# Optimization experiments

Measured on AMD Instinct MI355X. Metric: run time of the kernel, lower is better.

The kernel has to match this reference:

```python
import jax, jax.numpy as jnp
import numpy as np

HEADS = 8
DIM_HEAD = 64
INNER = HEADS * DIM_HEAD  # 512
EPS = 1e-6


def layer_norm(x, gamma, beta):
    mu = jnp.mean(x, axis=-1, keepdims=True)
    var = jnp.var(x, axis=-1, keepdims=True)
    return (x - mu) * jax.lax.rsqrt(var + EPS) * gamma + beta


def setup_inputs() -> dict:
    key = jax.random.key(0)
    ks = jax.random.split(key, 8)
    b, n = 2, 2048
    s = lambda d: 1.0 / np.sqrt(d)
    return {
        "x": jax.random.normal(ks[0], (b, n, INNER), dtype=jnp.float32),
        # weights stored input-major: y = x @ W
        "w_qkv": jax.random.normal(ks[1], (INNER, 3 * INNER), dtype=jnp.float32) * s(INNER),
        "w_out": jax.random.normal(ks[2], (INNER, INNER), dtype=jnp.float32) * s(INNER),
        "b_out": jax.random.normal(ks[3], (INNER,), dtype=jnp.float32) * 0.01,
        "w_ff1": jax.random.normal(ks[4], (INNER, 4 * INNER), dtype=jnp.float32) * s(INNER),
        "w_ff2": jax.random.normal(ks[5], (4 * INNER, INNER), dtype=jnp.float32) * s(4 * INNER),
        "g1": jnp.ones((INNER,), dtype=jnp.float32),
        "be1": jnp.zeros((INNER,), dtype=jnp.float32),
        "g2": jnp.ones((INNER,), dtype=jnp.float32),
        "be2": jnp.zeros((INNER,), dtype=jnp.float32),
    }


def reference(x, w_qkv, w_out, b_out, w_ff1, w_ff2, g1, be1, g2, be2):
    b, n, _ = x.shape
    scale = DIM_HEAD ** (-0.5)
    qkv = x @ w_qkv  # [b, n, 3*inner]
    qkv = qkv.reshape(b, n, 3, HEADS, DIM_HEAD)
    q = qkv[:, :, 0].transpose(0, 2, 1, 3)  # [b, h, n, d]
    k = qkv[:, :, 1].transpose(0, 2, 1, 3)
    v = qkv[:, :, 2].transpose(0, 2, 1, 3)
    dots = jnp.einsum('bhqd,bhkd->bhqk', q, k) * scale
    attn = jax.nn.softmax(dots, axis=-1)
    out = jnp.einsum('bhqk,bhkd->bhqd', attn, v)
    out = out.transpose(0, 2, 1, 3).reshape(b, n, INNER)
    out = out @ w_out + b_out
    attn_res = layer_norm(x + out, g1, be1)
    # NOTE: no activation between the two FFN linears (faithful to source)
    ff = (attn_res @ w_ff1) @ w_ff2
    return layer_norm(attn_res + ff, g2, be2)
```

## Files before the change

### kernel.cpp

```cpp
#include <hip/hip_runtime.h>
#include <hip/hip_bf16.h>
#include <cstdint>
#include <cstddef>
#include <math.h>

#define HEADS 8
#define DHEAD 64
#define INNER 512
#define BATCH 2
#define SEQ   2048
#define MROWS (BATCH*SEQ)
#define LN_EPS 1e-6f
#define KSPLIT 4
#define KCHUNK (SEQ/KSPLIT)

typedef unsigned short u16;
typedef __attribute__((ext_vector_type(8))) short short8;
typedef __attribute__((ext_vector_type(4))) short short4v;
typedef __attribute__((ext_vector_type(4))) float f32x4;

#define MFMA16(a,b,c) __builtin_amdgcn_mfma_f32_16x16x32_bf16((a),(b),(c),0,0,0)
#if __has_builtin(__builtin_amdgcn_mfma_f32_16x16x16bf16_1k)
#define HAVE_MFMA16K16 1
#define MFMA16K16(a,b,c) __builtin_amdgcn_mfma_f32_16x16x16bf16_1k((a),(b),(c),0,0,0)
#endif

__device__ __forceinline__ float bf2f(u16 u) {
    union { float f; uint32_t i; } x; x.i = ((uint32_t)u) << 16; return x.f;
}
__device__ __forceinline__ u16 f2bf(float f) {
    __hip_bfloat16 h = __float2bfloat16(f);
    return *reinterpret_cast<u16*>(&h);
}
__device__ __forceinline__ void gl_lds16(const void* g, void* l) {
    __builtin_amdgcn_global_load_lds(
        (const __attribute__((address_space(1))) void*)g,
        (__attribute__((address_space(3))) void*)l, 16, 0, 0);
}

__global__ void prep_kernel(const float* __restrict__ x, u16* __restrict__ x_b,
                            const float* __restrict__ w_qkv, u16* __restrict__ w_qkvT,
                            const float* __restrict__ w_out, u16* __restrict__ w_outT,
                            const float* __restrict__ w_ff1, u16* __restrict__ w_ff1T,
                            const float* __restrict__ w_ff2, u16* __restrict__ w_ff2T) {
    __shared__ float T[32][33];
    const int blk = blockIdx.x, tid = threadIdx.x;
    if (blk < 2048) {
        int i = blk * 256 + tid;
        float4 v = reinterpret_cast<const float4*>(x)[i];
        ushort4 o;
        o.x = f2bf(v.x); o.y = f2bf(v.y); o.z = f2bf(v.z); o.w = f2bf(v.w);
        reinterpret_cast<ushort4*>(x_b)[i] = o;
        return;
    }
    const float* B; u16* Bt; int K, N, t;
    if (blk < 2816)      { B = w_qkv; Bt = w_qkvT; K = 512;  N = 1536; t = blk - 2048; }
    else if (blk < 3072) { B = w_out; Bt = w_outT; K = 512;  N = 512;  t = blk - 2816; }
    else if (blk < 4096) { B = w_ff1; Bt = w_ff1T; K = 512;  N = 2048; t = blk - 3072; }
    else                 { B = w_ff2; Bt = w_ff2T; K = 2048; N = 512;  t = blk - 4096; }
    const int nb = N / 32;
    const int n0 = (t % nb) * 32, k0 = (t / nb) * 32;
    const int r = tid >> 3, c = (tid & 7) * 4;
    float4 v = *reinterpret_cast<const float4*>(&B[(size_t)(k0 + r) * N + n0 + c]);
    T[c + 0][r] = v.x; T[c + 1][r] = v.y; T[c + 2][r] = v.z; T[c + 3][r] = v.w;
    __syncthreads();
    ushort4 o;
    o.x = f2bf(T[r][c + 0]); o.y = f2bf(T[r][c + 1]);
    o.z = f2bf(T[r][c + 2]); o.w = f2bf(T[r][c + 3]);
    *reinterpret_cast<ushort4*>(&Bt[(size_t)(n0 + r) * K + k0 + c]) = o;
}

template<int BN, int EPI>
__global__ __launch_bounds__(256) void gemm_bt(const u16* __restrict__ A,
                                               const u16* __restrict__ Bt,
                                               u16* __restrict__ Cb,
                                               u16* __restrict__ Vt,
                                               int M, int N, int K) {
    constexpr int WN = BN / 2;
    constexpr int NT = WN / 16;
    __shared__ u16 As[128 * 32];
    __shared__ u16 Bs[BN * 32];
    const int tid = threadIdx.x;
    const int wave = tid >> 6, lane = tid & 63;
    const int l15 = lane & 15, quad = lane >> 4;
    const int wm = (wave >> 1) * 64, wn = (wave & 1) * WN;
    const int row0 = blockIdx.y * 128, col0 = blockIdx.x * BN;

    int kbase = 0, kend = K;
    if (EPI == 3) {
        int chunk = K / gridDim.z;
        kbase = blockIdx.z * chunk; kend = kbase + chunk;
    }

    f32x4 acc[4][NT];
    #pragma unroll
    for (int mi = 0; mi < 4; ++mi)
        #pragma unroll
        for (int ni = 0; ni < NT; ++ni)
            #pragma unroll
            for (int e = 0; e < 4; ++e) acc[mi][ni][e] = 0.f;

    for (int k0 = kbase; k0 < kend; k0 += 32) {
        #pragma unroll
        for (int idx0 = 0; idx0 < 512 + BN * 4; idx0 += 256) {
            int idx = idx0 + tid;
            if (idx < 512) {
                int r = idx >> 2, ic = (idx & 3) * 8;
                gl_lds16(A + (size_t)(row0 + r) * K + k0 + ic, &As[idx * 8]);
            } else {
                int ib = idx - 512;
                int r = ib >> 2, ic = (ib & 3) * 8;
                gl_lds16(Bt + (size_t)(col0 + r) * K + k0 + ic, &Bs[ib * 8]);
            }
        }
        __syncthreads();

        short8 af[4], bfr[NT];
        #pragma unroll
        for (int mi = 0; mi < 4; ++mi)
            af[mi] = *reinterpret_cast<const short8*>(&As[(wm + mi * 16 + l15) * 32 + quad * 8]);
        #pragma unroll
        for (int ni = 0; ni < NT; ++ni)
            bfr[ni] = *reinterpret_cast<const short8*>(&Bs[(wn + ni * 16 + l15) * 32 + quad * 8]);
        #pragma unroll
        for (int mi = 0; mi < 4; ++mi)
            #pragma unroll
            for (int ni = 0; ni < NT; ++ni)
                acc[mi][ni] = MFMA16(af[mi], bfr[ni], acc[mi][ni]);
        __syncthreads();
    }

    #pragma unroll
    for (int mi = 0; mi < 4; ++mi)
        #pragma unroll
        for (int ni = 0; ni < NT; ++ni) {
            const int cc = col0 + wn + ni * 16 + l15;
            const int rr0 = row0 + wm + mi * 16 + quad * 4;
            if (EPI == 0) {
                #pragma unroll
                for (int r = 0; r < 4; ++r)
                    Cb[(size_t)(rr0 + r) * N + cc] = f2bf(acc[mi][ni][r]);
            } else if (EPI == 3) {
                u16* Cz = Cb + (size_t)blockIdx.z * M * N;
                #pragma unroll
                for (int r = 0; r < 4; ++r)
                    Cz[(size_t)(rr0 + r) * N + cc] = f2bf(acc[mi][ni][r]);
            } else {
                if (cc < 1024) {
                    size_t base = (cc < 512) ? (size_t)cc
                                             : ((size_t)MROWS * 512 + cc - 512);
                    #pragma unroll
                    for (int r = 0; r < 4; ++r)
                        Cb[base + (size_t)(rr0 + r) * 512] = f2bf(acc[mi][ni][r]);
                } else {
                    int hh = (cc - 1024) >> 6, dd = (cc - 1024) & 63;
                    int bb = rr0 >> 11, srow = rr0 & 2047;
                    ushort4 o;
                    o.x = f2bf(acc[mi][ni][0]); o.y = f2bf(acc[mi][ni][1]);
                    o.z = f2bf(acc[mi][ni][2]); o.w = f2bf(acc[mi][ni][3]);
                    *reinterpret_cast<ushort4*>(
                        &Vt[(((size_t)(bb * 8 + hh) * 64 + dd) << 11) + srow]) = o;
                }
            }
        }
}

__global__ __launch_bounds__(256) void gemm_proj(const u16* __restrict__ OpartB,
                                                 const float* __restrict__ lpart,
                                                 const u16* __restrict__ Bt,
                                                 const float* __restrict__ bias,
                                                 float* __restrict__ C) {
    __shared__ u16 As[64 * 32];
    __shared__ u16 Bs[64 * 32];
    const int tid = threadIdx.x;
    const int wave = tid >> 6, lane = tid & 63;
    const int l15 = lane & 15, quad = lane >> 4;
    const int wm = (wave >> 1) * 32, wn = (wave & 1) * 32;
    const int row0 = blockIdx.y * 64, col0 = blockIdx.x * 64;

    f32x4 acc[2][2];
    #pragma unroll
    for (int mi = 0; mi < 2; ++mi)
        #pragma unroll
        for (int ni = 0; ni < 2; ++ni)
            #pragma unroll
            for (int e = 0; e < 4; ++e) acc[mi][ni][e] = 0.f;

    const int r = tid >> 2, ic = (tid & 3) * 8;
    const int gr = row0 + r;
    const int bb = gr >> 11, srow = gr & 2047;

    for (int k0 = 0; k0 < 512; k0 += 32) {
        gl_lds16(Bt + (size_t)(col0 + r) * 512 + k0 + ic, &Bs[tid * 8]);
        {
            const int gc = k0 + ic;
            const int h = gc >> 6, d0 = gc & 63;
            const int bh = bb * 8 + h;
            float l = 0.f, o[8] = {0.f, 0.f, 0.f, 0.f, 0.f, 0.f, 0.f, 0.f};
            #pragma unroll
            for (int ks = 0; ks < KSPLIT; ++ks) {
                size_t pk = ((size_t)(ks * 16 + bh) << 11) + srow;
                l += lpart[pk];
                uint4 uv = *reinterpret_cast<const uint4*>(&OpartB[pk * 64 + d0]);
                const u16* up = (const u16*)&uv;
                #pragma unroll
                for (int i = 0; i < 8; ++i) o[i] += bf2f(up[i]);
            }
            float inv = 1.f / l;
            u16 a8[8];
            #pragma unroll
            for (int i = 0; i < 8; ++i) a8[i] = f2bf(o[i] * inv);
            *reinterpret_cast<uint4*>(&As[tid * 8]) =
                *reinterpret_cast<const uint4*>(a8);
        }
        __syncthreads();

        short8 af[2], bfr[2];
        #pragma unroll
        for (int mi = 0; mi < 2; ++mi)
            af[mi] = *reinterpret_cast<const short8*>(&As[(wm + mi * 16 + l15) * 32 + quad * 8]);
        #pragma unroll
        for (int ni = 0; ni < 2; ++ni)
            bfr[ni] = *reinterpret_cast<const short8*>(&Bs[(wn + ni * 16 + l15) * 32 + quad * 8]);
        #pragma unroll
        for (int mi = 0; mi < 2; ++mi)
            #pragma unroll
            for (int ni = 0; ni < 2; ++ni)
                acc[mi][ni] = MFMA16(af[mi], bfr[ni], acc[mi][ni]);
        __syncthreads();
    }

    #pragma unroll
    for (int mi = 0; mi < 2; ++mi)
        #pragma unroll
        for (int ni = 0; ni < 2; ++ni) {
            const int cc = col0 + wn + ni * 16 + l15;
            const int rr0 = row0 + wm + mi * 16 + quad * 4;
            #pragma unroll
            for (int rr = 0; rr < 4; ++rr)
                C[(size_t)(rr0 + rr) * 512 + cc] = acc[mi][ni][rr] + bias[cc];
        }
}

__global__ __launch_bounds__(256) void attn_kernel(const u16* __restrict__ qk_b,
                                                   const u16* __restrict__ vT_b,
                                                   u16* __restrict__ OpartB,
                                                   float* __restrict__ lpart) {
    __shared__ u16 SM[64 * 64 + 2 * 64 * 72];
    u16 (*Qs)[64] = (u16(*)[64])SM;
    u16 (*Ks)[72] = (u16(*)[72])(SM + 64 * 64);
    u16 (*VT)[72] = (u16(*)[72])(SM + 64 * 64 + 64 * 72);

    const int tid = threadIdx.x;
    const int wave = tid >> 6, lane = tid & 63;
    const int l15 = lane & 15, quad = lane >> 4;
    const int qt = blockIdx.x, bh = blockIdx.y, ks = blockIdx.z;
    const int b = bh >> 3, h = bh & 7;
    const int w16 = wave * 16;
    const int r0 = tid >> 3, r1 = r0 + 32;
    const int ch = (tid & 7) * 8;

    {
        const u16* qb = qk_b + (size_t)(b * SEQ + qt * 64) * 512 + h * 64;
        *reinterpret_cast<uint4*>(&Qs[r0][ch]) =
            *reinterpret_cast<const uint4*>(&qb[(size_t)r0 * 512 + ch]);
        *reinterpret_cast<uint4*>(&Qs[r1][ch]) =
            *reinterpret_cast<const uint4*>(&qb[(size_t)r1 * 512 + ch]);
    }
    __syncthreads();

    short8 qf[2];
    qf[0] = *reinterpret_cast<const short8*>(&Qs[w16 + l15][quad * 8]);
    qf[1] = *reinterpret_cast<const short8*>(&Qs[w16 + l15][32 + quad * 8]);

    const u16* kb = qk_b + (size_t)MROWS * 512
                  + (size_t)(b * SEQ + ks * KCHUNK) * 512 + h * 64;
    const u16* vb = vT_b + (size_t)bh * 64 * 2048 + ks * KCHUNK;

    uint4 kr0 = *reinterpret_cast<const uint4*>(&kb[(size_t)r0 * 512 + ch]);
    uint4 kr1 = *reinterpret_cast<const uint4*>(&kb[(size_t)r1 * 512 + ch]);
    uint4 vr0 = *reinterpret_cast<const uint4*>(&vb[(size_t)r0 * 2048 + ch]);
    uint4 vr1 = *reinterpret_cast<const uint4*>(&vb[(size_t)r1 * 2048 + ch]);

    const float CEXP = 0.18033688011110918f;

#ifdef HAVE_MFMA16K16
    f32x4 oacc[4];
    float lsum = 0.f;
    #pragma unroll
    for (int di = 0; di < 4; ++di)
        #pragma unroll
        for (int e = 0; e < 4; ++e) oacc[di][e] = 0.f;

    for (int kt = 0; kt < KCHUNK / 64; ++kt) {
        *reinterpret_cast<uint4*>(&Ks[r0][ch]) = kr0;
        *reinterpret_cast<uint4*>(&Ks[r1][ch]) = kr1;
        *reinterpret_cast<uint4*>(&VT[r0][ch]) = vr0;
        *reinterpret_cast<uint4*>(&VT[r1][ch]) = vr1;
        __syncthreads();

        if (kt + 1 < KCHUNK / 64) {
            const u16* kb2 = kb + (size_t)(kt + 1) * 64 * 512;
            const u16* vb2 = vb + (kt + 1) * 64;
            kr0 = *reinterpret_cast<const uint4*>(&kb2[(size_t)r0 * 512 + ch]);
            kr1 = *reinterpret_cast<const uint4*>(&kb2[(size_t)r1 * 512 + ch]);
            vr0 = *reinterpret_cast<const uint4*>(&vb2[(size_t)r0 * 2048 + ch]);
            vr1 = *reinterpret_cast<const uint4*>(&vb2[(size_t)r1 * 2048 + ch]);
        }

        f32x4 sacc[4];
        #pragma unroll
        for (int ni = 0; ni < 4; ++ni)
            #pragma unroll
            for (int e = 0; e < 4; ++e) sacc[ni][e] = 0.f;
        #pragma unroll
        for (int ksk = 0; ksk < 2; ++ksk) {
            short8 kf[4];
            #pragma unroll
            for (int ni = 0; ni < 4; ++ni)
                kf[ni] = *reinterpret_cast<const short8*>(
                    &Ks[ni * 16 + l15][ksk * 32 + quad * 8]);
            #pragma unroll
            for (int ni = 0; ni < 4; ++ni)
                sacc[ni] = MFMA16(kf[ni], qf[ksk], sacc[ni]);
        }

        #pragma unroll
        for (int ni = 0; ni < 4; ++ni) {
            short4v pp;
            #pragma unroll
            for (int r = 0; r < 4; ++r) {
                float p = exp2f(sacc[ni][r] * CEXP);
                lsum += p;
                pp[r] = (short)f2bf(p);
            }
            #pragma unroll
            for (int di = 0; di < 4; ++di) {
                short4v vf = *reinterpret_cast<const short4v*>(
                    &VT[di * 16 + l15][ni * 16 + quad * 4]);
                oacc[di] = MFMA16K16(vf, pp, oacc[di]);
            }
        }
        __syncthreads();
    }

    lsum += __shfl_xor(lsum, 16);
    lsum += __shfl_xor(lsum, 32);

    const size_t pbase = ((size_t)(ks * 16 + bh) * SEQ + qt * 64);
    if (lane < 16) lpart[pbase + w16 + lane] = lsum;

    float* OTf = (float*)SM;
    #pragma unroll
    for (int di = 0; di < 4; ++di)
        #pragma unroll
        for (int r = 0; r < 4; ++r)
            OTf[(di * 16 + quad * 4 + r) * 68 + w16 + l15] = oacc[di][r];
    __syncthreads();

    const int ql = tid >> 2, dseg = (tid & 3) * 16;
    u16 ov[16];
    #pragma unroll
    for (int i = 0; i < 16; ++i) ov[i] = f2bf(OTf[(dseg + i) * 68 + ql]);
    u16* op = &OpartB[(pbase + ql) * 64 + dseg];
    *reinterpret_cast<uint4*>(op)     = *reinterpret_cast<const uint4*>(ov);
    *reinterpret_cast<uint4*>(op + 8) = *reinterpret_cast<const uint4*>(ov + 8);
#else
    f32x4 oacc[4];
    float lsum[4];
    #pragma unroll
    for (int di = 0; di < 4; ++di)
        #pragma unroll
        for (int e = 0; e < 4; ++e) oacc[di][e] = 0.f;
    #pragma unroll
    for (int r = 0; r < 4; ++r) lsum[r] = 0.f;

    for (int kt = 0; kt < KCHUNK / 64; ++kt) {
        *reinterpret_cast<uint4*>(&Ks[r0][ch]) = kr0;
        *reinterpret_cast<uint4*>(&Ks[r1][ch]) = kr1;
        *reinterpret_cast<uint4*>(&VT[r0][ch]) = vr0;
        *reinterpret_cast<uint4*>(&VT[r1][ch]) = vr1;
        __syncthreads();

        if (kt + 1 < KCHUNK / 64) {
            const u16* kb2 = kb + (size_t)(kt + 1) * 64 * 512;
            const u16* vb2 = vb + (kt + 1) * 64;
            kr0 = *reinterpret_cast<const uint4*>(&kb2[(size_t)r0 * 512 + ch]);
            kr1 = *reinterpret_cast<const uint4*>(&kb2[(size_t)r1 * 512 + ch]);
            vr0 = *reinterpret_cast<const uint4*>(&vb2[(size_t)r0 * 2048 + ch]);
            vr1 = *reinterpret_cast<const uint4*>(&vb2[(size_t)r1 * 2048 + ch]);
        }

        f32x4 sacc[4];
        #pragma unroll
        for (int ni = 0; ni < 4; ++ni)
            #pragma unroll
            for (int e = 0; e < 4; ++e) sacc[ni][e] = 0.f;
        #pragma unroll
        for (int ksk = 0; ksk < 2; ++ksk) {
            short8 kf[4];
            #pragma unroll
            for (int ni = 0; ni < 4; ++ni)
                kf[ni] = *reinterpret_cast<const short8*>(
                    &Ks[ni * 16 + l15][ksk * 32 + quad * 8]);
            #pragma unroll
            for (int ni = 0; ni < 4; ++ni)
                sacc[ni] = MFMA16(qf[ksk], kf[ni], sacc[ni]);
        }
        #pragma unroll
        for (int ni = 0; ni < 4; ++ni)
            #pragma unroll
            for (int r = 0; r < 4; ++r) {
                float p = exp2f(sacc[ni][r] * CEXP);
                lsum[r] += p;
                Qs[w16 + quad * 4 + r][ni * 16 + l15] = f2bf(p);
            }
        #pragma unroll
        for (int ksk = 0; ksk < 2; ++ksk) {
            short8 pf = *reinterpret_cast<const short8*>(
                &Qs[w16 + l15][ksk * 32 + quad * 8]);
            #pragma unroll
            for (int di = 0; di < 4; ++di) {
                short8 vf = *reinterpret_cast<const short8*>(
                    &VT[di * 16 + l15][ksk * 32 + quad * 8]);
                oacc[di] = MFMA16(pf, vf, oacc[di]);
            }
        }
        __syncthreads();
    }

    #pragma unroll
    for (int r = 0; r < 4; ++r) {
        float v = lsum[r];
        v += __shfl_xor(v, 1); v += __shfl_xor(v, 2);
        v += __shfl_xor(v, 4); v += __shfl_xor(v, 8);
        lsum[r] = v;
    }
    const size_t pbase = ((size_t)(ks * 16 + bh) * SEQ + qt * 64);
    #pragma unroll
    for (int di = 0; di < 4; ++di)
        #pragma unroll
        for (int r = 0; r < 4; ++r)
            OpartB[(pbase + w16 + quad * 4 + r) * 64 + di * 16 + l15] = f2bf(oacc[di][r]);
    if (l15 == 0)
        #pragma unroll
        for (int r = 0; r < 4; ++r)
            lpart[pbase + w16 + quad * 4 + r] = lsum[r];
#endif
}

template<bool A16, bool S16, bool TWO>
__global__ __launch_bounds__(256) void ln_kernel(const void* __restrict__ a_,
                                                 const void* __restrict__ s0_,
                                                 const void* __restrict__ s1_,
                                                 const float* __restrict__ g,
                                                 const float* __restrict__ be,
                                                 float* __restrict__ out32,
                                                 u16* __restrict__ out16) {
    const int tid = threadIdx.x, wave = tid >> 6, lane = tid & 63;
    const int row = blockIdx.x * 4 + wave;
    const size_t off = (size_t)row * INNER;

    float v[8];
    #pragma unroll
    for (int j = 0; j < 2; ++j) {
        const int c = j * 256 + lane * 4;
        float a0, a1, a2, a3;
        if (A16) {
            ushort4 u = *reinterpret_cast<const ushort4*>((const u16*)a_ + off + c);
            a0 = bf2f(u.x); a1 = bf2f(u.y); a2 = bf2f(u.z); a3 = bf2f(u.w);
        } else {
            float4 u = *reinterpret_cast<const float4*>((const float*)a_ + off + c);
            a0 = u.x; a1 = u.y; a2 = u.z; a3 = u.w;
        }
        float s0, s1, s2, s3;
        if (S16) {
            ushort4 u = *reinterpret_cast<const ushort4*>((const u16*)s0_ + off + c);
            s0 = bf2f(u.x); s1 = bf2f(u.y); s2 = bf2f(u.z); s3 = bf2f(u.w);
        } else {
            float4 u = *reinterpret_cast<const float4*>((const float*)s0_ + off + c);
            s0 = u.x; s1 = u.y; s2 = u.z; s3 = u.w;
        }
        v[j*4+0] = a0 + s0; v[j*4+1] = a1 + s1; v[j*4+2] = a2 + s2; v[j*4+3] = a3 + s3;
        if (TWO) {
            if (S16) {
                ushort4 u = *reinterpret_cast<const ushort4*>((const u16*)s1_ + off + c);
                v[j*4+0] += bf2f(u.x); v[j*4+1] += bf2f(u.y);
                v[j*4+2] += bf2f(u.z); v[j*4+3] += bf2f(u.w);
            } else {
                float4 u = *reinterpret_cast<const float4*>((const float*)s1_ + off + c);
                v[j*4+0] += u.x; v[j*4+1] += u.y; v[j*4+2] += u.z; v[j*4+3] += u.w;
            }
        }
    }

    float s = 0.f;
    #pragma unroll
    for (int i = 0; i < 8; ++i) s += v[i];
    #pragma unroll
    for (int m = 1; m < 64; m <<= 1) s += __shfl_xor(s, m);
    const float mu = s * (1.f / INNER);

    float q = 0.f;
    #pragma unroll
    for (int i = 0; i < 8; ++i) { v[i] -= mu; q += v[i] * v[i]; }
    #pragma unroll
    for (int m = 1; m < 64; m <<= 1) q += __shfl_xor(q, m);
    const float rstd = rsqrtf(q * (1.f / INNER) + LN_EPS);

    #pragma unroll
    for (int j = 0; j < 2; ++j) {
        const int c = j * 256 + lane * 4;
        float4 gv = *reinterpret_cast<const float4*>(g + c);
        float4 bv = *reinterpret_cast<const float4*>(be + c);
        float y0 = v[j*4+0] * rstd * gv.x + bv.x;
        float y1 = v[j*4+1] * rstd * gv.y + bv.y;
        float y2 = v[j*4+2] * rstd * gv.z + bv.z;
        float y3 = v[j*4+3] * rstd * gv.w + bv.w;
        if (out32) {
            float4 o = {y0, y1, y2, y3};
            *reinterpret_cast<float4*>(out32 + off + c) = o;
        }
        if (out16) {
            ushort4 o;
            o.x = f2bf(y0); o.y = f2bf(y1); o.z = f2bf(y2); o.w = f2bf(y3);
            *reinterpret_cast<ushort4*>(out16 + off + c) = o;
        }
    }
}

extern "C" void kernel_launch(void* const* d_in, const int* in_sizes, int n_in,
                              void* d_out, int out_size, void* d_ws, size_t ws_size,
                              hipStream_t stream) {
    const float* x     = (const float*)d_in[0];
    const float* w_qkv = (const float*)d_in[1];
    const float* w_out = (const float*)d_in[2];
    const float* b_out = (const float*)d_in[3];
    const float* w_ff1 = (const float*)d_in[4];
    const float* w_ff2 = (const float*)d_in[5];
    const float* g1    = (const float*)d_in[6];
    const float* be1   = (const float*)d_in[7];
    const float* g2    = (const float*)d_in[8];
    const float* be2   = (const float*)d_in[9];
    float* out = (float*)d_out;

    char* W = (char*)d_ws;
    u16*   w_outT     = (u16*)  (W + 0);
    u16*   w_ff1T     = (u16*)  (W + 524288);
    u16*   w_ff2T     = (u16*)  (W + 2621440);
    u16*   qk_b       = (u16*)  (W + 4718592);
    float* proj       = (float*)(W + 4718592);
    u16*   ff2p       = (u16*)  (W + 4718592);
    u16*   vT_b       = (u16*)  (W + 13107200);
    u16*   attn_res_b = (u16*)  (W + 13107200);
    u16*   x_b        = (u16*)  (W + 17301504);
    u16*   w_qkvT     = (u16*)  (W + 21495808);
    u16*   OpartB     = (u16*)  (W + 17301504);
    u16*   ff1_b      = (u16*)  (W + 17301504);
    float* lpart      = (float*)(W + 34078720);

    prep_kernel<<<5120, 256, 0, stream>>>(x, x_b, w_qkv, w_qkvT, w_out, w_outT,
                                          w_ff1, w_ff1T, w_ff2, w_ff2T);

    gemm_bt<64, 2><<<dim3(1536 / 64, MROWS / 128), 256, 0, stream>>>(
        x_b, w_qkvT, qk_b, vT_b, MROWS, 1536, INNER);

    attn_kernel<<<dim3(SEQ / 64, BATCH * HEADS, KSPLIT), 256, 0, stream>>>(
        qk_b, vT_b, OpartB, lpart);

    gemm_proj<<<dim3(INNER / 64, MROWS / 64), 256, 0, stream>>>(
        OpartB, lpart, w_outT, b_out, proj);

    ln_kernel<false, false, false><<<MROWS / 4, 256, 0, stream>>>(
        x, proj, nullptr, g1, be1, nullptr, attn_res_b);

    gemm_bt<128, 0><<<dim3(2048 / 128, MROWS / 128), 256, 0, stream>>>(
        attn_res_b, w_ff1T, ff1_b, nullptr, MROWS, 2048, INNER);

    gemm_bt<64, 3><<<dim3(INNER / 64, MROWS / 128, 2), 256, 0, stream>>>(
        ff1_b, w_ff2T, ff2p, nullptr, MROWS, INNER, 2048);

    ln_kernel<true, true, true><<<MROWS / 4, 256, 0, stream>>>(
        attn_res_b, ff2p, ff2p + (size_t)MROWS * INNER, g2, be2, out, nullptr);
}
```

Baseline: 233.1 us.

## Fold softmax scale into Q, split attention combine from output projection

Pre-multiplies Q by the softmax scale (log2e/sqrt(d)) in the QKV GEMM epilogue, so the attention kernel's exp2 no longer needs a multiply. The P-to-bf16 pack now uses byte-permute truncation, which rounds toward zero instead of to nearest. The fused combine+projection kernel, which recomputed the split-K merge for every column tile, becomes a separate elementwise combine kernel plus the generic 128-row GEMM with a bias epilogue. This adds a kernel launch and an extra bf16 intermediate round-trip, and slightly changes numerics.

```diff
diff --git a/kernel.cpp b/kernel.cpp
--- a/kernel.cpp
+++ b/kernel.cpp
@@ -13,6 +13,7 @@
 #define LN_EPS 1e-6f
 #define KSPLIT 4
 #define KCHUNK (SEQ/KSPLIT)
+#define QSCALE 0.18033688011110918f
 
 typedef unsigned short u16;
 typedef __attribute__((ext_vector_type(8))) short short8;
@@ -73,6 +74,8 @@
 template<int BN, int EPI>
 __global__ __launch_bounds__(256) void gemm_bt(const u16* __restrict__ A,
                                                const u16* __restrict__ Bt,
+                                               const float* __restrict__ bias,
+                                               float* __restrict__ C,
                                                u16* __restrict__ Cb,
                                                u16* __restrict__ Vt,
                                                int M, int N, int K) {
@@ -140,6 +143,10 @@
                 #pragma unroll
                 for (int r = 0; r < 4; ++r)
                     Cb[(size_t)(rr0 + r) * N + cc] = f2bf(acc[mi][ni][r]);
+            } else if (EPI == 1) {
+                #pragma unroll
+                for (int r = 0; r < 4; ++r)
+                    C[(size_t)(rr0 + r) * N + cc] = acc[mi][ni][r] + bias[cc];
             } else if (EPI == 3) {
                 u16* Cz = Cb + (size_t)blockIdx.z * M * N;
                 #pragma unroll
@@ -147,11 +154,13 @@
                     Cz[(size_t)(rr0 + r) * N + cc] = f2bf(acc[mi][ni][r]);
             } else {
                 if (cc < 1024) {
-                    size_t base = (cc < 512) ? (size_t)cc
-                                             : ((size_t)MROWS * 512 + cc - 512);
+                    const bool isq = (cc < 512);
+                    size_t base = isq ? (size_t)cc
+                                      : ((size_t)MROWS * 512 + cc - 512);
+                    const float sc = isq ? QSCALE : 1.f;
                     #pragma unroll
                     for (int r = 0; r < 4; ++r)
-                        Cb[base + (size_t)(rr0 + r) * 512] = f2bf(acc[mi][ni][r]);
+                        Cb[base + (size_t)(rr0 + r) * 512] = f2bf(acc[mi][ni][r] * sc);
                 } else {
                     int hh = (cc - 1024) >> 6, dd = (cc - 1024) & 63;
                     int bb = rr0 >> 11, srow = rr0 & 2047;
@@ -165,83 +174,6 @@
         }
 }
 
-__global__ __launch_bounds__(256) void gemm_proj(const u16* __restrict__ OpartB,
-                                                 const float* __restrict__ lpart,
-                                                 const u16* __restrict__ Bt,
-                                                 const float* __restrict__ bias,
-                                                 float* __restrict__ C) {
-    __shared__ u16 As[64 * 32];
-    __shared__ u16 Bs[64 * 32];
-    const int tid = threadIdx.x;
-    const int wave = tid >> 6, lane = tid & 63;
-    const int l15 = lane & 15, quad = lane >> 4;
-    const int wm = (wave >> 1) * 32, wn = (wave & 1) * 32;
-    const int row0 = blockIdx.y * 64, col0 = blockIdx.x * 64;
-
-    f32x4 acc[2][2];
-    #pragma unroll
-    for (int mi = 0; mi < 2; ++mi)
-        #pragma unroll
-        for (int ni = 0; ni < 2; ++ni)
-            #pragma unroll
-            for (int e = 0; e < 4; ++e) acc[mi][ni][e] = 0.f;
-
-    const int r = tid >> 2, ic = (tid & 3) * 8;
-    const int gr = row0 + r;
-    const int bb = gr >> 11, srow = gr & 2047;
-
-    for (int k0 = 0; k0 < 512; k0 += 32) {
-        gl_lds16(Bt + (size_t)(col0 + r) * 512 + k0 + ic, &Bs[tid * 8]);
-        {
-            const int gc = k0 + ic;
-            const int h = gc >> 6, d0 = gc & 63;
-            const int bh = bb * 8 + h;
-            float l = 0.f, o[8] = {0.f, 0.f, 0.f, 0.f, 0.f, 0.f, 0.f, 0.f};
-            #pragma unroll
-            for (int ks = 0; ks < KSPLIT; ++ks) {
-                size_t pk = ((size_t)(ks * 16 + bh) << 11) + srow;
-                l += lpart[pk];
-                uint4 uv = *reinterpret_cast<const uint4*>(&OpartB[pk * 64 + d0]);
-                const u16* up = (const u16*)&uv;
-                #pragma unroll
-                for (int i = 0; i < 8; ++i) o[i] += bf2f(up[i]);
-            }
-            float inv = 1.f / l;
-            u16 a8[8];
-            #pragma unroll
-            for (int i = 0; i < 8; ++i) a8[i] = f2bf(o[i] * inv);
-            *reinterpret_cast<uint4*>(&As[tid * 8]) =
-                *reinterpret_cast<const uint4*>(a8);
-        }
-        __syncthreads();
-
-        short8 af[2], bfr[2];
-        #pragma unroll
-        for (int mi = 0; mi < 2; ++mi)
-            af[mi] = *reinterpret_cast<const short8*>(&As[(wm + mi * 16 + l15) * 32 + quad * 8]);
-        #pragma unroll
-        for (int ni = 0; ni < 2; ++ni)
-            bfr[ni] = *reinterpret_cast<const short8*>(&Bs[(wn + ni * 16 + l15) * 32 + quad * 8]);
-        #pragma unroll
-        for (int mi = 0; mi < 2; ++mi)
-            #pragma unroll
-            for (int ni = 0; ni < 2; ++ni)
-                acc[mi][ni] = MFMA16(af[mi], bfr[ni], acc[mi][ni]);
-        __syncthreads();
-    }
-
-    #pragma unroll
-    for (int mi = 0; mi < 2; ++mi)
-        #pragma unroll
-        for (int ni = 0; ni < 2; ++ni) {
-            const int cc = col0 + wn + ni * 16 + l15;
-            const int rr0 = row0 + wm + mi * 16 + quad * 4;
-            #pragma unroll
-            for (int rr = 0; rr < 4; ++rr)
-                C[(size_t)(rr0 + rr) * 512 + cc] = acc[mi][ni][rr] + bias[cc];
-        }
-}
-
 __global__ __launch_bounds__(256) void attn_kernel(const u16* __restrict__ qk_b,
                                                    const u16* __restrict__ vT_b,
                                                    u16* __restrict__ OpartB,
@@ -282,8 +214,6 @@
     uint4 vr0 = *reinterpret_cast<const uint4*>(&vb[(size_t)r0 * 2048 + ch]);
     uint4 vr1 = *reinterpret_cast<const uint4*>(&vb[(size_t)r1 * 2048 + ch]);
 
-    const float CEXP = 0.18033688011110918f;
-
 #ifdef HAVE_MFMA16K16
     f32x4 oacc[4];
     float lsum = 0.f;
@@ -327,18 +257,21 @@
 
         #pragma unroll
         for (int ni = 0; ni < 4; ++ni) {
-            short4v pp;
-            #pragma unroll
-            for (int r = 0; r < 4; ++r) {
-                float p = exp2f(sacc[ni][r] * CEXP);
-                lsum += p;
-                pp[r] = (short)f2bf(p);
-            }
+            float p0 = exp2f(sacc[ni][0]);
+            float p1 = exp2f(sacc[ni][1]);
+            float p2 = exp2f(sacc[ni][2]);
+            float p3 = exp2f(sacc[ni][3]);
+            lsum += (p0 + p1) + (p2 + p3);
+            union { short4v v; uint32_t u[2]; } P;
+            P.u[0] = __builtin_amdgcn_perm(__float_as_uint(p1),
+                                           __float_as_uint(p0), 0x07060302u);
+            P.u[1] = __builtin_amdgcn_perm(__float_as_uint(p3),
+                                           __float_as_uint(p2), 0x07060302u);
             #pragma unroll
             for (int di = 0; di < 4; ++di) {
                 short4v vf = *reinterpret_cast<const short4v*>(
                     &VT[di * 16 + l15][ni * 16 + quad * 4]);
-                oacc[di] = MFMA16K16(vf, pp, oacc[di]);
+                oacc[di] = MFMA16K16(vf, P.v, oacc[di]);
             }
         }
         __syncthreads();
@@ -411,7 +344,7 @@
         for (int ni = 0; ni < 4; ++ni)
             #pragma unroll
             for (int r = 0; r < 4; ++r) {
-                float p = exp2f(sacc[ni][r] * CEXP);
+                float p = exp2f(sacc[ni][r]);
                 lsum[r] += p;
                 Qs[w16 + quad * 4 + r][ni * 16 + l15] = f2bf(p);
             }
@@ -447,6 +380,32 @@
         for (int r = 0; r < 4; ++r)
             lpart[pbase + w16 + quad * 4 + r] = lsum[r];
 #endif
+}
+
+__global__ void attn_combine_kernel(const u16* __restrict__ OpartB,
+                                    const float* __restrict__ lpart,
+                                    u16* __restrict__ attn_b) {
+    int i = blockIdx.x * 256 + threadIdx.x;
+    int e = i * 4;
+    int row = e >> 9;
+    int c = e & 511;
+    int h = c >> 6, d = c & 63;
+    int b = row >> 11, srow = row & 2047;
+    int bh = b * 8 + h;
+
+    float ax = 0.f, ay = 0.f, az = 0.f, aw = 0.f, l = 0.f;
+    #pragma unroll
+    for (int ks = 0; ks < KSPLIT; ++ks) {
+        size_t pk = (size_t)(ks * 16 + bh) * SEQ + srow;
+        ushort4 o = *reinterpret_cast<const ushort4*>(&OpartB[pk * 64 + d]);
+        ax += bf2f(o.x); ay += bf2f(o.y); az += bf2f(o.z); aw += bf2f(o.w);
+        l += lpart[pk];
+    }
+    float li = 1.f / l;
+    ushort4 o;
+    o.x = f2bf(ax * li); o.y = f2bf(ay * li);
+    o.z = f2bf(az * li); o.w = f2bf(aw * li);
+    *reinterpret_cast<ushort4*>(&attn_b[(size_t)row * INNER + c]) = o;
 }
 
 template<bool A16, bool S16, bool TWO>
@@ -558,27 +517,31 @@
     u16*   OpartB     = (u16*)  (W + 17301504);
     u16*   ff1_b      = (u16*)  (W + 17301504);
     float* lpart      = (float*)(W + 34078720);
+    u16*   attn_b     = (u16*)  (W + 34603008);
 
     prep_kernel<<<5120, 256, 0, stream>>>(x, x_b, w_qkv, w_qkvT, w_out, w_outT,
                                           w_ff1, w_ff1T, w_ff2, w_ff2T);
 
     gemm_bt<64, 2><<<dim3(1536 / 64, MROWS / 128), 256, 0, stream>>>(
-        x_b, w_qkvT, qk_b, vT_b, MROWS, 1536, INNER);
+        x_b, w_qkvT, nullptr, nullptr, qk_b, vT_b, MROWS, 1536, INNER);
 
     attn_kernel<<<dim3(SEQ / 64, BATCH * HEADS, KSPLIT), 256, 0, stream>>>(
         qk_b, vT_b, OpartB, lpart);
 
-    gemm_proj<<<dim3(INNER / 64, MROWS / 64), 256, 0, stream>>>(
-        OpartB, lpart, w_outT, b_out, proj);
+    attn_combine_kernel<<<(MROWS * INNER / 4) / 256, 256, 0, stream>>>(
+        OpartB, lpart, attn_b);
+
+    gemm_bt<64, 1><<<dim3(INNER / 64, MROWS / 128), 256, 0, stream>>>(
+        attn_b, w_outT, b_out, proj, nullptr, nullptr, MROWS, INNER, INNER);
 
     ln_kernel<false, false, false><<<MROWS / 4, 256, 0, stream>>>(
         x, proj, nullptr, g1, be1, nullptr, attn_res_b);
 
     gemm_bt<128, 0><<<dim3(2048 / 128, MROWS / 128), 256, 0, stream>>>(
-        attn_res_b, w_ff1T, ff1_b, nullptr, MROWS, 2048, INNER);
+        attn_res_b, w_ff1T, nullptr, nullptr, ff1_b, nullptr, MROWS, 2048, INNER);
 
     gemm_bt<64, 3><<<dim3(INNER / 64, MROWS / 128, 2), 256, 0, stream>>>(
-        ff1_b, w_ff2T, ff2p, nullptr, MROWS, INNER, 2048);
+        ff1_b, w_ff2T, nullptr, nullptr, ff2p, nullptr, MROWS, INNER, 2048);
 
     ln_kernel<true, true, true><<<MROWS / 4, 256, 0, stream>>>(
         attn_res_b, ff2p, ff2p + (size_t)MROWS * INNER, g2, be2, out, nullptr);
```

Measured after the change: 211.0 us. 9.5% less time.
